# Kernel tuning notes

Measured on AMD Instinct MI355X. Metric: run time of the kernel, lower is better.

## Reference

```python
import jax, jax.numpy as jnp
import numpy as np

N_NODES = 20000
N_EDGES = 320000  # directed edges, in reverse pairs (2*i, 2*i+1)
F_NODE = 64
F_EDGE = 16
HID = 300
DEPTH = 3
N_GRAPHS = 128


def setup_inputs() -> dict:
    key = jax.random.key(0)
    ks = jax.random.split(key, 16)
    x = jax.random.normal(ks[0], (N_NODES, F_NODE), dtype=jnp.float32)
    edge_attr = jax.random.normal(ks[1], (N_EDGES, F_EDGE), dtype=jnp.float32)
    # build paired directed edges: edge 2*i is (src,dst), edge 2*i+1 is (dst,src)
    half = N_EDGES // 2
    src = jax.random.randint(ks[2], (half,), 0, N_NODES)
    dst = jax.random.randint(ks[3], (half,), 0, N_NODES)
    row = jnp.stack([src, dst], axis=1).reshape(-1)  # [E]
    col = jnp.stack([dst, src], axis=1).reshape(-1)  # [E]
    edge_index = jnp.stack([row, col], axis=0)  # [2, E]
    batch = jnp.sort(jax.random.randint(ks[4], (N_NODES,), 0, N_GRAPHS))
    s = 0.05
    W_init = jax.random.normal(ks[5], (F_NODE + F_EDGE, HID), dtype=jnp.float32) * s
    b_init = jnp.zeros((HID,), dtype=jnp.float32)
    W_convs = jax.random.normal(ks[6], (DEPTH, HID, HID), dtype=jnp.float32) * s
    b_convs = jnp.zeros((DEPTH, HID), dtype=jnp.float32)
    W_e2n = jax.random.normal(ks[7], (F_NODE + HID, HID), dtype=jnp.float32) * s
    b_e2n = jnp.zeros((HID,), dtype=jnp.float32)
    W_ffn = jax.random.normal(ks[8], (HID, 1), dtype=jnp.float32) * s
    b_ffn = jnp.zeros((1,), dtype=jnp.float32)
    return {"x": x, "edge_attr": edge_attr, "edge_index": edge_index, "batch": batch,
            "W_init": W_init, "b_init": b_init, "W_convs": W_convs, "b_convs": b_convs,
            "W_e2n": W_e2n, "b_e2n": b_e2n, "W_ffn": W_ffn, "b_ffn": b_ffn}


def _rev(h):
    # swap each consecutive forward/reverse edge pair
    e = h.shape[0]
    return h.reshape(e // 2, 2, -1)[:, ::-1, :].reshape(e, -1)


def reference(x, edge_attr, edge_index, batch, W_init, b_init, W_convs, b_convs,
              W_e2n, b_e2n, W_ffn, b_ffn):
    row, col = edge_index[0], edge_index[1]
    # h_0 = act(edge_init(cat([x[row], edge_attr])))
    h0 = jax.nn.relu(jnp.concatenate([x[row], edge_attr], axis=1) @ W_init + b_init)
    h = h0
    for l in range(DEPTH):
        # DMPNNConv: scatter-add edge features to target nodes, gather at source,
        # subtract reverse-edge message, apply Linear
        a = jax.ops.segment_sum(h, col, num_segments=N_NODES)  # [N, H]
        h = (a[row] - _rev(h)) @ W_convs[l] + b_convs[l]
        h = jax.nn.relu(h + h0)  # skip then activation; dropout is eval no-op
    # final conv's a_message only
    s = jax.ops.segment_sum(h, col, num_segments=N_NODES)  # [N, H]
    q = jnp.concatenate([x, s], axis=1)
    hn = jax.nn.relu(q @ W_e2n + b_e2n)  # [N, H]
    pooled = jax.ops.segment_sum(hn, batch, num_segments=N_GRAPHS)  # [G, H]
    return (pooled @ W_ffn + b_ffn).squeeze(-1)  # [G]
```

## Files before the change

kernel.cpp:

```cpp
#include <hip/hip_runtime.h>
#include <hip/hip_bf16.h>

typedef unsigned short ushort_t;
typedef __attribute__((ext_vector_type(8))) short short8;
typedef __attribute__((ext_vector_type(4))) float f32x4;
typedef __attribute__((ext_vector_type(2))) float f32x2;

#define N_NODES 20000
#define N_EDGES 320000
#define F_NODE 64
#define F_EDGE 16
#define HID 300
#define HP 300
#define NTILES 20
#define DEPTH 3
#define N_GRAPHS 128
#define KE2N 384
#define ATS 328

#define WFRAG_USHORT_PER_LAYER (10 * NTILES * 64 * 8)
#define W2FRAG_USHORT (NTILES * 64 * 8)
#define WE2NFRAG_USHORT (12 * NTILES * 64 * 8)

__device__ __forceinline__ float bf2f(ushort_t u) {
    union { unsigned int i; float f; } v;
    v.i = ((unsigned int)u) << 16;
    return v.f;
}

__device__ __forceinline__ f32x2 bfpair(unsigned int u) {
    union { unsigned int i[2]; f32x2 f; } v;
    v.i[0] = u << 16;
    v.i[1] = u & 0xffff0000u;
    return v.f;
}

__device__ __forceinline__ f32x2 pmax0(f32x2 a) {
#if __has_builtin(__builtin_elementwise_max)
    f32x2 z = {0.f, 0.f};
    return __builtin_elementwise_max(a, z);
#else
    f32x2 r; r.x = fmaxf(a.x, 0.f); r.y = fmaxf(a.y, 0.f); return r;
#endif
}

__device__ __forceinline__ unsigned int fpack(float lo, float hi) {
#if __has_builtin(__builtin_amdgcn_cvt_pk_bf16_f32)
    auto r = __builtin_amdgcn_cvt_pk_bf16_f32(lo, hi);
    union { decltype(r) b; unsigned int u; } v;
    v.b = r;
    return v.u;
#else
    union { float f; unsigned int i; } a, b;
    a.f = lo; b.f = hi;
    return ((a.i + 0x8000u) >> 16) | ((b.i + 0x8000u) & 0xffff0000u);
#endif
}
__device__ __forceinline__ unsigned int fpack2(f32x2 a) { return fpack(a.x, a.y); }
__device__ __forceinline__ ushort_t f2bf(float f) {
    return (ushort_t)(fpack(f, 0.f) & 0xffffu);
}

__global__ __launch_bounds__(256) void csr_hist(
    const int* __restrict__ col, int* __restrict__ deg)
{
    int e = blockIdx.x * 256 + threadIdx.x;
    atomicAdd(&deg[col[e]], 1);
}

__global__ __launch_bounds__(256) void csr_scan(
    const int* __restrict__ deg, int* __restrict__ offsets,
    int* __restrict__ cursor)
{
    __shared__ int sums[256];
    const int t = threadIdx.x;
    const int CH = 79;
    int base = t * CH;
    int local = 0;
    for (int i = 0; i < CH; ++i) {
        int idx = base + i;
        if (idx < N_NODES) local += deg[idx];
    }
    sums[t] = local;
    __syncthreads();
    for (int off = 1; off < 256; off <<= 1) {
        int v = (t >= off) ? sums[t - off] : 0;
        __syncthreads();
        sums[t] += v;
        __syncthreads();
    }
    int run = (t > 0) ? sums[t - 1] : 0;
    for (int i = 0; i < CH; ++i) {
        int idx = base + i;
        if (idx < N_NODES) {
            offsets[idx] = run;
            cursor[idx] = run;
            run += deg[idx];
        }
    }
}

__global__ __launch_bounds__(256) void csr_fill(
    const int* __restrict__ col, int* __restrict__ cursor,
    int* __restrict__ eid)
{
    int e = blockIdx.x * 256 + threadIdx.x;
    int pos = atomicAdd(&cursor[col[e]], 1);
    eid[pos] = e;
}

__global__ __launch_bounds__(256) void ghist(
    const int* __restrict__ batch, int* __restrict__ gdeg)
{
    int n = blockIdx.x * 256 + threadIdx.x;
    if (n < N_NODES) atomicAdd(&gdeg[batch[n]], 1);
}

__global__ __launch_bounds__(128) void gscan(
    const int* __restrict__ gdeg, int* __restrict__ goff)
{
    __shared__ int s[128];
    int t = threadIdx.x;
    int d = gdeg[t];
    s[t] = d;
    __syncthreads();
    for (int off = 1; off < 128; off <<= 1) {
        int v = (t >= off) ? s[t - off] : 0;
        __syncthreads();
        s[t] += v;
        __syncthreads();
    }
    goff[t] = s[t] - d;
    if (t == 127) goff[128] = s[127];
}

__global__ __launch_bounds__(64) void wfrag_build(
    const float* __restrict__ W_convs, ushort_t* __restrict__ wfrag)
{
    const int c = blockIdx.x, t = blockIdx.y, l = blockIdx.z;
    const int lane = threadIdx.x;
    const int k0 = c * 32 + (lane >> 4) * 8;
    const int n  = t * 16 + (lane & 15);
    ushort_t* dst = wfrag + (size_t)l * WFRAG_USHORT_PER_LAYER
                  + ((size_t)(c * NTILES + t) * 64 + lane) * 8;
    const float* Wl = W_convs + (size_t)l * HID * HID;
    #pragma unroll
    for (int j = 0; j < 8; ++j) {
        int k = k0 + j;
        float v = (k < HID && n < HID) ? Wl[(long)k * HID + n] : 0.f;
        dst[j] = f2bf(v);
    }
}

__global__ __launch_bounds__(64) void wfrag2_build(
    const float* __restrict__ W_e2n, ushort_t* __restrict__ wfrag2)
{
    const int c = blockIdx.x, t = blockIdx.y;
    const int lane = threadIdx.x;
    const int k0 = c * 32 + (lane >> 4) * 8;
    const int n  = t * 16 + (lane & 15);
    ushort_t* dst = wfrag2 + ((size_t)(c * NTILES + t) * 64 + lane) * 8;
    #pragma unroll
    for (int j = 0; j < 8; ++j) {
        int k = k0 + j;
        float v = (k < F_NODE + HID && n < HID) ? W_e2n[(long)k * HID + n] : 0.f;
        dst[j] = f2bf(v);
    }
}

__global__ __launch_bounds__(64) void w2frag_build(
    const float* __restrict__ W2, ushort_t* __restrict__ w2frag)
{
    const int t = blockIdx.x;
    const int lane = threadIdx.x;
    const int k0 = (lane >> 4) * 8;
    const int n  = t * 16 + (lane & 15);
    ushort_t* dst = w2frag + ((size_t)t * 64 + lane) * 8;
    #pragma unroll
    for (int j = 0; j < 8; ++j) {
        int k = k0 + j;
        float v = (k < F_EDGE && n < HID) ? W2[(long)k * HID + n] : 0.f;
        dst[j] = f2bf(v);
    }
}


__global__ __launch_bounds__(256) void node_init_gemm(
    const float* __restrict__ x, const float* __restrict__ W_init,
    const float* __restrict__ b_init, ushort_t* __restrict__ xW1b)
{
    __shared__ float xs[16 * 64];
    const int tid = threadIdx.x;
    const long n0 = (long)blockIdx.x * 16;
    for (int i = tid; i < 16 * 64; i += 256) xs[i] = x[n0 * 64 + i];
    __syncthreads();
    const int nl = tid >> 4, ct = tid & 15;
    for (int q = 0; q < 19; ++q) {
        int c = ct + 16 * q;
        if (c < HID) {
            float acc = b_init[c];
            #pragma unroll 8
            for (int k = 0; k < 64; ++k)
                acc = fmaf(xs[nl * 64 + k], W_init[(long)k * HID + c], acc);
            xW1b[(n0 + nl) * HID + c] = f2bf(acc);
        }
    }
}

template<bool UPDATE>
__global__ __launch_bounds__(256) void fused_conv(
    ushort_t* h, const ushort_t* __restrict__ Sb,
    const ushort_t* __restrict__ xW1b, const float* __restrict__ edge_attr,
    const int* __restrict__ row, const ushort_t* __restrict__ w2frag,
    const ushort_t* __restrict__ wfrag_l)
{
    __shared__ ushort_t At[32 * ATS];
    __shared__ int rows[32];
    const int tid = threadIdx.x;
    const int wave = tid >> 6, lane = tid & 63;
    const int quad = lane >> 4, m = lane & 15;
    const long e0 = (long)blockIdx.x * 32;
    if (tid < 32) rows[tid] = row[e0 + tid];

    {
        short8 a_ea[2];
        #pragma unroll
        for (int mt = 0; mt < 2; ++mt) {
            union { uint4 u4; short8 s8; } af;
            if (quad < 2) {
                const float* eap = edge_attr + (e0 + mt * 16 + m) * 16 + quad * 8;
                float4 v0 = *(const float4*)eap;
                float4 v1 = *(const float4*)(eap + 4);
                af.u4.x = fpack(v0.x, v0.y); af.u4.y = fpack(v0.z, v0.w);
                af.u4.z = fpack(v1.x, v1.y); af.u4.w = fpack(v1.z, v1.w);
            } else {
                af.u4.x = 0; af.u4.y = 0; af.u4.z = 0; af.u4.w = 0;
            }
            a_ea[mt] = af.s8;
        }
        const int nt0 = wave * 5;
        #pragma unroll
        for (int t = 0; t < 5; ++t) {
            short8 b = *(const short8*)(w2frag + ((size_t)(nt0 + t) * 64 + lane) * 8);
            int c = (nt0 + t) * 16 + m;
            #pragma unroll
            for (int mt = 0; mt < 2; ++mt) {
                f32x4 pc = (f32x4){0.f, 0.f, 0.f, 0.f};
                pc = __builtin_amdgcn_mfma_f32_16x16x32_bf16(a_ea[mt], b, pc, 0, 0, 0);
                #pragma unroll
                for (int r = 0; r < 4; ++r)
                    At[(mt * 16 + quad * 4 + r) * ATS + c] = f2bf(pc[r]);
            }
        }
    }
    __syncthreads();

    for (int i = tid; i < 16 * 80; i += 256) {
        int p = i / 80, g = i % 80;
        int c0 = 4 * g;
        int la = 2 * p, lb = 2 * p + 1;
        uint2 oa, ob;
        if (g < 75) {
            long Ea = e0 + la, Eb = e0 + lb;
            int ra = rows[la], rb = rows[lb];
            uint2 xa = *(const uint2*)&xW1b[(long)ra * HID + c0];
            uint2 xb = *(const uint2*)&xW1b[(long)rb * HID + c0];
            uint2 pa = *(const uint2*)&At[la * ATS + c0];
            uint2 pb = *(const uint2*)&At[lb * ATS + c0];
            f32x2 h0a0 = pmax0(bfpair(xa.x) + bfpair(pa.x));
            f32x2 h0a1 = pmax0(bfpair(xa.y) + bfpair(pa.y));
            f32x2 h0b0 = pmax0(bfpair(xb.x) + bfpair(pb.x));
            f32x2 h0b1 = pmax0(bfpair(xb.y) + bfpair(pb.y));
            if (UPDATE) {
                uint2 wa = *(const uint2*)&h[Ea * HP + c0];
                uint2 wb = *(const uint2*)&h[Eb * HP + c0];
                uint2 sa = *(const uint2*)&Sb[(long)ra * HID + c0];
                uint2 sb = *(const uint2*)&Sb[(long)rb * HID + c0];
                oa.x = fpack2(pmax0(bfpair(sa.x) - bfpair(wb.x) + h0a0));
                oa.y = fpack2(pmax0(bfpair(sa.y) - bfpair(wb.y) + h0a1));
                ob.x = fpack2(pmax0(bfpair(sb.x) - bfpair(wa.x) + h0b0));
                ob.y = fpack2(pmax0(bfpair(sb.y) - bfpair(wa.y) + h0b1));
            } else {
                oa.x = fpack2(h0a0); oa.y = fpack2(h0a1);
                ob.x = fpack2(h0b0); ob.y = fpack2(h0b1);
            }
        } else {
            oa.x = 0; oa.y = 0;
            ob = oa;
        }
        *(uint2*)&At[la * ATS + c0] = oa;
        *(uint2*)&At[lb * ATS + c0] = ob;
    }
    __syncthreads();

    const int nt0 = wave * 5;
    f32x4 acc[5][2];
    #pragma unroll
    for (int t = 0; t < 5; ++t)
        #pragma unroll
        for (int mt = 0; mt < 2; ++mt)
            acc[t][mt] = (f32x4){0.f, 0.f, 0.f, 0.f};

    for (int c = 0; c < 10; ++c) {
        short8 a[2];
        #pragma unroll
        for (int mt = 0; mt < 2; ++mt)
            a[mt] = *(const short8*)&At[(mt * 16 + m) * ATS + c * 32 + quad * 8];
        #pragma unroll
        for (int t = 0; t < 5; ++t) {
            short8 b = *(const short8*)(wfrag_l
                + ((size_t)(c * NTILES + nt0 + t) * 64 + lane) * 8);
            #pragma unroll
            for (int mt = 0; mt < 2; ++mt)
                acc[t][mt] = __builtin_amdgcn_mfma_f32_16x16x32_bf16(
                    a[mt], b, acc[t][mt], 0, 0, 0);
        }
    }
    #pragma unroll
    for (int t = 0; t < 5; ++t) {
        int col = (nt0 + t) * 16 + m;
        if (col >= HID) continue;
        #pragma unroll
        for (int mt = 0; mt < 2; ++mt) {
            long rbase = (e0 + mt * 16 + quad * 4) * HP + col;
            #pragma unroll
            for (int r = 0; r < 4; ++r)
                h[rbase + (long)r * HP] = f2bf(acc[t][mt][r]);
        }
    }
}

__global__ __launch_bounds__(256) void edge_update_mfma(
    ushort_t* h, const ushort_t* __restrict__ Sb,
    const ushort_t* __restrict__ xW1b, const float* __restrict__ edge_attr,
    const int* __restrict__ row, const ushort_t* __restrict__ w2frag)
{
    __shared__ ushort_t Pt[32 * ATS];
    __shared__ int rows[32];
    const int tid = threadIdx.x;
    const int wave = tid >> 6, lane = tid & 63;
    const int quad = lane >> 4, m = lane & 15;
    const long e0 = (long)blockIdx.x * 32;
    if (tid < 32) rows[tid] = row[e0 + tid];

    {
        short8 a_ea[2];
        #pragma unroll
        for (int mt = 0; mt < 2; ++mt) {
            union { uint4 u4; short8 s8; } af;
            if (quad < 2) {
                const float* eap = edge_attr + (e0 + mt * 16 + m) * 16 + quad * 8;
                float4 v0 = *(const float4*)eap;
                float4 v1 = *(const float4*)(eap + 4);
                af.u4.x = fpack(v0.x, v0.y); af.u4.y = fpack(v0.z, v0.w);
                af.u4.z = fpack(v1.x, v1.y); af.u4.w = fpack(v1.z, v1.w);
            } else {
                af.u4.x = 0; af.u4.y = 0; af.u4.z = 0; af.u4.w = 0;
            }
            a_ea[mt] = af.s8;
        }
        const int nt0 = wave * 5;
        #pragma unroll
        for (int t = 0; t < 5; ++t) {
            short8 b = *(const short8*)(w2frag + ((size_t)(nt0 + t) * 64 + lane) * 8);
            #pragma unroll
            for (int mt = 0; mt < 2; ++mt) {
                f32x4 pc = (f32x4){0.f, 0.f, 0.f, 0.f};
                pc = __builtin_amdgcn_mfma_f32_16x16x32_bf16(a_ea[mt], b, pc, 0, 0, 0);
                int c = (nt0 + t) * 16 + m;
                #pragma unroll
                for (int r = 0; r < 4; ++r)
                    Pt[(mt * 16 + quad * 4 + r) * ATS + c] = f2bf(pc[r]);
            }
        }
    }
    __syncthreads();

    for (int i = tid; i < 16 * 75; i += 256) {
        int p = i / 75, g = i % 75;
        int c0 = 4 * g;
        int la = 2 * p, lb = 2 * p + 1;
        long Ea = e0 + la, Eb = e0 + lb;
        int ra = rows[la], rb = rows[lb];
        uint2 wa = *(const uint2*)&h[Ea * HP + c0];
        uint2 wb = *(const uint2*)&h[Eb * HP + c0];
        uint2 sa = *(const uint2*)&Sb[(long)ra * HID + c0];
        uint2 sb = *(const uint2*)&Sb[(long)rb * HID + c0];
        uint2 xa = *(const uint2*)&xW1b[(long)ra * HID + c0];
        uint2 xb = *(const uint2*)&xW1b[(long)rb * HID + c0];
        uint2 pa = *(const uint2*)&Pt[la * ATS + c0];
        uint2 pb = *(const uint2*)&Pt[lb * ATS + c0];
        f32x2 h0a0 = pmax0(bfpair(xa.x) + bfpair(pa.x));
        f32x2 h0a1 = pmax0(bfpair(xa.y) + bfpair(pa.y));
        f32x2 h0b0 = pmax0(bfpair(xb.x) + bfpair(pb.x));
        f32x2 h0b1 = pmax0(bfpair(xb.y) + bfpair(pb.y));
        uint2 oa, ob;
        oa.x = fpack2(pmax0(bfpair(sa.x) - bfpair(wb.x) + h0a0));
        oa.y = fpack2(pmax0(bfpair(sa.y) - bfpair(wb.y) + h0a1));
        ob.x = fpack2(pmax0(bfpair(sb.x) - bfpair(wa.x) + h0b0));
        ob.y = fpack2(pmax0(bfpair(sb.y) - bfpair(wa.y) + h0b1));
        *(uint2*)&h[Ea * HP + c0] = oa;
        *(uint2*)&h[Eb * HP + c0] = ob;
    }
}

__global__ __launch_bounds__(256) void gather_sum(
    const ushort_t* __restrict__ src, const int* __restrict__ offsets,
    const int* __restrict__ ends, const int* __restrict__ eid,
    const float* __restrict__ bias, ushort_t* __restrict__ Sb)
{
    long idx = (long)blockIdx.x * 256 + threadIdx.x;
    if (idx >= (long)N_NODES * 75) return;
    int n = (int)(idx / 75);
    int g = (int)(idx % 75);
    int beg = offsets[n], end = ends[n];
    f32x2 A0 = {0.f, 0.f}, A1 = {0.f, 0.f};
    f32x2 B0 = {0.f, 0.f}, B1 = {0.f, 0.f};
    int j = beg;
    for (; j + 1 < end; j += 2) {
        int e0i = eid[j], e1i = eid[j + 1];
        uint2 v0 = ((const uint2*)src)[(long)e0i * (HP / 4) + g];
        uint2 v1 = ((const uint2*)src)[(long)e1i * (HP / 4) + g];
        A0 += bfpair(v0.x); A1 += bfpair(v0.y);
        B0 += bfpair(v1.x); B1 += bfpair(v1.y);
    }
    if (j < end) {
        int e0i = eid[j];
        uint2 v0 = ((const uint2*)src)[(long)e0i * (HP / 4) + g];
        A0 += bfpair(v0.x); A1 += bfpair(v0.y);
    }
    float4 bv = *(const float4*)&bias[4 * g];
    f32x2 bv0 = {bv.x, bv.y}, bv1 = {bv.z, bv.w};
    uint2 o;
    o.x = fpack2(A0 + B0 + bv0);
    o.y = fpack2(A1 + B1 + bv1);
    *(uint2*)&Sb[(long)n * HID + 4 * g] = o;
}

__global__ __launch_bounds__(256) void gather_ab(
    const ushort_t* __restrict__ src, const int* __restrict__ offsets,
    const int* __restrict__ ends, const int* __restrict__ eid,
    ushort_t* __restrict__ Ab)
{
    long idx = (long)blockIdx.x * 256 + threadIdx.x;
    if (idx >= (long)N_NODES * 75) return;
    int n = (int)(idx / 75);
    int g = (int)(idx % 75);
    int beg = offsets[n], end = ends[n];
    f32x2 A0 = {0.f, 0.f}, A1 = {0.f, 0.f};
    f32x2 B0 = {0.f, 0.f}, B1 = {0.f, 0.f};
    int j = beg;
    for (; j + 1 < end; j += 2) {
        int e0i = eid[j], e1i = eid[j + 1];
        uint2 v0 = ((const uint2*)src)[(long)e0i * (HP / 4) + g];
        uint2 v1 = ((const uint2*)src)[(long)e1i * (HP / 4) + g];
        A0 += bfpair(v0.x); A1 += bfpair(v0.y);
        B0 += bfpair(v1.x); B1 += bfpair(v1.y);
    }
    if (j < end) {
        int e0i = eid[j];
        uint2 v0 = ((const uint2*)src)[(long)e0i * (HP / 4) + g];
        A0 += bfpair(v0.x); A1 += bfpair(v0.y);
    }
    uint2 o;
    o.x = fpack2(A0 + B0);
    o.y = fpack2(A1 + B1);
    *(uint2*)&Ab[(long)n * KE2N + 64 + 4 * g] = o;
}

__global__ __launch_bounds__(256) void x_fill(
    const float* __restrict__ x, ushort_t* __restrict__ Ab)
{
    long idx = (long)blockIdx.x * 256 + threadIdx.x;
    if (idx >= (long)N_NODES * 21) return;
    int n = (int)(idx / 21);
    int q = (int)(idx % 21);
    if (q < 16) {
        float4 v = *(const float4*)&x[(long)n * 64 + 4 * q];
        uint2 o;
        o.x = fpack(v.x, v.y);
        o.y = fpack(v.z, v.w);
        *(uint2*)&Ab[(long)n * KE2N + 4 * q] = o;
    } else {
        uint2 o; o.x = 0; o.y = 0;
        *(uint2*)&Ab[(long)n * KE2N + 364 + 4 * (q - 16)] = o;
    }
}

__global__ __launch_bounds__(256) void e2n_mfma(
    const ushort_t* __restrict__ Ab, const ushort_t* __restrict__ wfrag2,
    const float* __restrict__ b_e2n, float* __restrict__ hn)
{
    const int tid = threadIdx.x;
    const int wave = tid >> 6, lane = tid & 63;
    const int quad = lane >> 4, m = lane & 15;
    const long n0 = (long)blockIdx.x * 64;
    const int nt0 = wave * 5;

    f32x4 acc[5][4];
    #pragma unroll
    for (int t = 0; t < 5; ++t)
        #pragma unroll
        for (int mt = 0; mt < 4; ++mt)
            acc[t][mt] = (f32x4){0.f, 0.f, 0.f, 0.f};

    for (int c = 0; c < 12; ++c) {
        short8 a[4];
        #pragma unroll
        for (int mt = 0; mt < 4; ++mt) {
            long r = n0 + mt * 16 + m;
            if (r > N_NODES - 1) r = N_NODES - 1;
            a[mt] = *(const short8*)(Ab + r * KE2N + c * 32 + quad * 8);
        }
        #pragma unroll
        for (int t = 0; t < 5; ++t) {
            short8 b = *(const short8*)(wfrag2
                + ((size_t)(c * NTILES + nt0 + t) * 64 + lane) * 8);
            #pragma unroll
            for (int mt = 0; mt < 4; ++mt)
                acc[t][mt] = __builtin_amdgcn_mfma_f32_16x16x32_bf16(
                    a[mt], b, acc[t][mt], 0, 0, 0);
        }
    }

    #pragma unroll
    for (int t = 0; t < 5; ++t) {
        int col = (nt0 + t) * 16 + m;
        if (col >= HID) continue;
        float bias = b_e2n[col];
        #pragma unroll
        for (int mt = 0; mt < 4; ++mt) {
            long rw = n0 + mt * 16 + quad * 4;
            #pragma unroll
            for (int r = 0; r < 4; ++r) {
                long rowi = rw + r;
                if (rowi < N_NODES)
                    hn[rowi * HP + col] = fmaxf(acc[t][mt][r] + bias, 0.f);
            }
        }
    }
}

__global__ __launch_bounds__(256) void pool_graph(
    const float* __restrict__ hn, const int* __restrict__ goff,
    float* __restrict__ pooled)
{
    int g = blockIdx.x;
    int beg = goff[g], end = goff[g + 1];
    for (int c = threadIdx.x; c < HID; c += 256) {
        float acc = 0.f;
        for (int n = beg; n < end; ++n)
            acc += hn[(long)n * HP + c];
        pooled[(long)g * HID + c] = acc;
    }
}

__global__ __launch_bounds__(64) void ffn_out(
    const float* __restrict__ pooled, const float* __restrict__ W_ffn,
    const float* __restrict__ b_ffn, float* __restrict__ out)
{
    int g = blockIdx.x;
    int lane = threadIdx.x;
    float s = 0.f;
    for (int c = lane; c < HID; c += 64)
        s += pooled[(long)g * HID + c] * W_ffn[c];
    #pragma unroll
    for (int off = 32; off > 0; off >>= 1)
        s += __shfl_down(s, off, 64);
    if (lane == 0) out[g] = s + b_ffn[0];
}

extern "C" void kernel_launch(void* const* d_in, const int* in_sizes, int n_in,
                              void* d_out, int out_size, void* d_ws, size_t ws_size,
                              hipStream_t stream) {
    const float* x         = (const float*)d_in[0];
    const float* edge_attr = (const float*)d_in[1];
    const int*   edge_index= (const int*)d_in[2];
    const int*   batch     = (const int*)d_in[3];
    const float* W_init    = (const float*)d_in[4];
    const float* b_init    = (const float*)d_in[5];
    const float* W_convs   = (const float*)d_in[6];
    const float* b_convs   = (const float*)d_in[7];
    const float* W_e2n     = (const float*)d_in[8];
    const float* b_e2n     = (const float*)d_in[9];
    const float* W_ffn     = (const float*)d_in[10];
    const float* b_ffn     = (const float*)d_in[11];
    float* out = (float*)d_out;

    const int* row = edge_index;
    const int* col = edge_index + N_EDGES;
    const float* W2 = W_init + (size_t)F_NODE * HID;

    const size_t need = (size_t)N_EDGES * HP * 2
                      + (size_t)N_NODES * HID * 2
                      + (size_t)N_NODES * KE2N * 2
                      + (size_t)N_GRAPHS * HID * 4
                      + (size_t)N_NODES * 4 * 2 + (size_t)N_EDGES * 4
                      + (size_t)DEPTH * WFRAG_USHORT_PER_LAYER * 2
                      + (size_t)WE2NFRAG_USHORT * 2
                      + (size_t)W2FRAG_USHORT * 2
                      + (size_t)(N_GRAPHS + 1 + N_GRAPHS) * 4 + 32768;
    if (ws_size < need) return;

    char* p = (char*)d_ws;
    auto take = [&](size_t bytes) {
        char* q = p;
        p += (bytes + 255) & ~(size_t)255;
        return q;
    };
    ushort_t* h       = (ushort_t*)take((size_t)N_EDGES * HP * 2);
    ushort_t* Sb      = (ushort_t*)take((size_t)N_NODES * HID * 2);
    ushort_t* Ab      = (ushort_t*)take((size_t)N_NODES * KE2N * 2);
    float*    pooled  = (float*)take((size_t)N_GRAPHS * HID * 4);
    int*      cursor  = (int*)take((size_t)N_NODES * 4);
    int*      offsets = (int*)take((size_t)N_NODES * 4);
    int*      eid     = (int*)take((size_t)N_EDGES * 4);
    ushort_t* wfrag   = (ushort_t*)take((size_t)DEPTH * WFRAG_USHORT_PER_LAYER * 2);
    ushort_t* wfrag2  = (ushort_t*)take((size_t)WE2NFRAG_USHORT * 2);
    ushort_t* w2frag  = (ushort_t*)take((size_t)W2FRAG_USHORT * 2);
    int*      gdeg    = (int*)take((size_t)N_GRAPHS * 4);
    int*      goff    = (int*)take((size_t)(N_GRAPHS + 1) * 4);

    ushort_t* xW1b = Ab;
    float*    hn   = (float*)h;

    hipMemsetAsync(cursor, 0, (size_t)N_NODES * 4, stream);
    hipMemsetAsync(gdeg, 0, (size_t)N_GRAPHS * 4, stream);
    csr_hist<<<N_EDGES / 256, 256, 0, stream>>>(col, cursor);
    csr_scan<<<1, 256, 0, stream>>>(cursor, offsets, cursor);
    csr_fill<<<N_EDGES / 256, 256, 0, stream>>>(col, cursor, eid);
    ghist<<<(N_NODES + 255) / 256, 256, 0, stream>>>(batch, gdeg);
    gscan<<<1, 128, 0, stream>>>(gdeg, goff);

    wfrag_build<<<dim3(10, NTILES, DEPTH), 64, 0, stream>>>(W_convs, wfrag);
    wfrag2_build<<<dim3(12, NTILES, 1), 64, 0, stream>>>(W_e2n, wfrag2);
    w2frag_build<<<NTILES, 64, 0, stream>>>(W2, w2frag);

    node_init_gemm<<<N_NODES / 16, 256, 0, stream>>>(x, W_init, b_init, xW1b);

    const int GS_GRID = ((N_NODES * 75) + 255) / 256;

    fused_conv<false><<<N_EDGES / 32, 256, 0, stream>>>(
        h, Sb, xW1b, edge_attr, row, w2frag, wfrag);
    gather_sum<<<GS_GRID, 256, 0, stream>>>(
        h, offsets, cursor, eid, b_convs + 0 * HID, Sb);
    fused_conv<true><<<N_EDGES / 32, 256, 0, stream>>>(
        h, Sb, xW1b, edge_attr, row, w2frag,
        wfrag + 1 * (size_t)WFRAG_USHORT_PER_LAYER);
    gather_sum<<<GS_GRID, 256, 0, stream>>>(
        h, offsets, cursor, eid, b_convs + 1 * HID, Sb);
    fused_conv<true><<<N_EDGES / 32, 256, 0, stream>>>(
        h, Sb, xW1b, edge_attr, row, w2frag,
        wfrag + 2 * (size_t)WFRAG_USHORT_PER_LAYER);
    gather_sum<<<GS_GRID, 256, 0, stream>>>(
        h, offsets, cursor, eid, b_convs + 2 * HID, Sb);
    edge_update_mfma<<<N_EDGES / 32, 256, 0, stream>>>(
        h, Sb, xW1b, edge_attr, row, w2frag);

    x_fill<<<((N_NODES * 21) + 255) / 256, 256, 0, stream>>>(x, Ab);
    gather_ab<<<GS_GRID, 256, 0, stream>>>(h, offsets, cursor, eid, Ab);
    e2n_mfma<<<(N_NODES + 63) / 64, 256, 0, stream>>>(Ab, wfrag2, b_e2n, hn);
    pool_graph<<<N_GRAPHS, 256, 0, stream>>>(hn, goff, pooled);
    ffn_out<<<N_GRAPHS, 64, 0, stream>>>(pooled, W_ffn, b_ffn, out);
}
```

Measured before the change: 1.233 ms.

## Software-pipeline gathers and MFMA operand loads; widen edge update and gather unroll

In fused_conv, the row/xW1b/h/Sb gathers for each elementwise iteration are issued one step ahead, and the first batch is issued before the edge-attr MFMA phase so its latency overlaps that compute. The main MFMA loop double-buffers its weight and LDS operand fragments. edge_update_mfma moves to 512 threads, using 8 waves for the edge-attr projection and the same prefetched gather scheme. The gather_sum and gather_ab kernels unroll their edge loops by 4 with separate accumulators to raise memory-level parallelism. The cost is higher register pressure, which could reduce occupancy.

```diff
diff --git a/kernel.cpp b/kernel.cpp
--- a/kernel.cpp
+++ b/kernel.cpp
@@ -207,6 +207,41 @@
     }
 }
 
+__device__ __forceinline__ void p_phase8(
+    ushort_t* At, const float* __restrict__ edge_attr,
+    const ushort_t* __restrict__ w2frag, long e0,
+    int wave, int quad, int m, int lane)
+{
+    const int mtp = wave >> 2;
+    const int nt0p = (wave & 3) * 5;
+    short8 a_ea;
+    {
+        union { uint4 u4; short8 s8; } af;
+        if (quad < 2) {
+            const float* eap = edge_attr + (e0 + mtp * 16 + m) * 16 + quad * 8;
+            float4 v0 = *(const float4*)eap;
+            float4 v1 = *(const float4*)(eap + 4);
+            af.u4.x = fpack(v0.x, v0.y); af.u4.y = fpack(v0.z, v0.w);
+            af.u4.z = fpack(v1.x, v1.y); af.u4.w = fpack(v1.z, v1.w);
+        } else {
+            af.u4.x = 0; af.u4.y = 0; af.u4.z = 0; af.u4.w = 0;
+        }
+        a_ea = af.s8;
+    }
+    #pragma unroll
+    for (int t = 0; t < 5; ++t) {
+        int nt = nt0p + t;
+        if (nt >= 19) continue;
+        short8 b = *(const short8*)(w2frag + ((size_t)nt * 64 + lane) * 8);
+        int c = nt * 16 + m;
+        f32x4 pc = (f32x4){0.f, 0.f, 0.f, 0.f};
+        pc = __builtin_amdgcn_mfma_f32_16x16x32_bf16(a_ea, b, pc, 0, 0, 0);
+        #pragma unroll
+        for (int r = 0; r < 4; ++r)
+            At[(mtp * 16 + quad * 4 + r) * ATS + c] = f2bf(pc[r]);
+    }
+}
+
 template<bool UPDATE>
 __global__ __launch_bounds__(256) void fused_conv(
     ushort_t* h, const ushort_t* __restrict__ Sb,
@@ -215,12 +250,33 @@
     const ushort_t* __restrict__ wfrag_l)
 {
     __shared__ ushort_t At[32 * ATS];
-    __shared__ int rows[32];
     const int tid = threadIdx.x;
     const int wave = tid >> 6, lane = tid & 63;
     const int quad = lane >> 4, m = lane & 15;
     const long e0 = (long)blockIdx.x * 32;
-    if (tid < 32) rows[tid] = row[e0 + tid];
+
+    auto issue = [&](int k, uint2& xa, uint2& xb, uint2& wa, uint2& wb,
+                     uint2& sa, uint2& sb, int& la, int& lb, int& g) {
+        int i = tid + (k << 8);
+        int p = i / 80; g = i % 80;
+        la = 2 * p; lb = la + 1;
+        if (g < 75) {
+            int c0 = 4 * g;
+            int ra = row[e0 + la], rb = row[e0 + lb];
+            xa = *(const uint2*)&xW1b[(long)ra * HID + c0];
+            xb = *(const uint2*)&xW1b[(long)rb * HID + c0];
+            if (UPDATE) {
+                wa = *(const uint2*)&h[(e0 + la) * HP + c0];
+                wb = *(const uint2*)&h[(e0 + lb) * HP + c0];
+                sa = *(const uint2*)&Sb[(long)ra * HID + c0];
+                sb = *(const uint2*)&Sb[(long)rb * HID + c0];
+            }
+        }
+    };
+
+    uint2 xa0, xb0, wa0, wb0, sa0, sb0;
+    int la0, lb0, g0;
+    issue(0, xa0, xb0, wa0, wb0, sa0, sb0, la0, lb0, g0);
 
     {
         short8 a_ea[2];
@@ -255,31 +311,26 @@
     }
     __syncthreads();
 
-    for (int i = tid; i < 16 * 80; i += 256) {
-        int p = i / 80, g = i % 80;
-        int c0 = 4 * g;
-        int la = 2 * p, lb = 2 * p + 1;
+    #pragma unroll
+    for (int k = 0; k < 5; ++k) {
+        uint2 xa1, xb1, wa1, wb1, sa1, sb1;
+        int la1 = 0, lb1 = 0, g1 = 0;
+        if (k < 4)
+            issue(k + 1, xa1, xb1, wa1, wb1, sa1, sb1, la1, lb1, g1);
+        int c0 = 4 * g0;
         uint2 oa, ob;
-        if (g < 75) {
-            long Ea = e0 + la, Eb = e0 + lb;
-            int ra = rows[la], rb = rows[lb];
-            uint2 xa = *(const uint2*)&xW1b[(long)ra * HID + c0];
-            uint2 xb = *(const uint2*)&xW1b[(long)rb * HID + c0];
-            uint2 pa = *(const uint2*)&At[la * ATS + c0];
-            uint2 pb = *(const uint2*)&At[lb * ATS + c0];
-            f32x2 h0a0 = pmax0(bfpair(xa.x) + bfpair(pa.x));
-            f32x2 h0a1 = pmax0(bfpair(xa.y) + bfpair(pa.y));
-            f32x2 h0b0 = pmax0(bfpair(xb.x) + bfpair(pb.x));
-            f32x2 h0b1 = pmax0(bfpair(xb.y) + bfpair(pb.y));
+        if (g0 < 75) {
+            uint2 pa = *(const uint2*)&At[la0 * ATS + c0];
+            uint2 pb = *(const uint2*)&At[lb0 * ATS + c0];
+            f32x2 h0a0 = pmax0(bfpair(xa0.x) + bfpair(pa.x));
+            f32x2 h0a1 = pmax0(bfpair(xa0.y) + bfpair(pa.y));
+            f32x2 h0b0 = pmax0(bfpair(xb0.x) + bfpair(pb.x));
+            f32x2 h0b1 = pmax0(bfpair(xb0.y) + bfpair(pb.y));
             if (UPDATE) {
-                uint2 wa = *(const uint2*)&h[Ea * HP + c0];
-                uint2 wb = *(const uint2*)&h[Eb * HP + c0];
-                uint2 sa = *(const uint2*)&Sb[(long)ra * HID + c0];
-                uint2 sb = *(const uint2*)&Sb[(long)rb * HID + c0];
-                oa.x = fpack2(pmax0(bfpair(sa.x) - bfpair(wb.x) + h0a0));
-                oa.y = fpack2(pmax0(bfpair(sa.y) - bfpair(wb.y) + h0a1));
-                ob.x = fpack2(pmax0(bfpair(sb.x) - bfpair(wa.x) + h0b0));
-                ob.y = fpack2(pmax0(bfpair(sb.y) - bfpair(wa.y) + h0b1));
+                oa.x = fpack2(pmax0(bfpair(sa0.x) - bfpair(wb0.x) + h0a0));
+                oa.y = fpack2(pmax0(bfpair(sa0.y) - bfpair(wb0.y) + h0a1));
+                ob.x = fpack2(pmax0(bfpair(sb0.x) - bfpair(wa0.x) + h0b0));
+                ob.y = fpack2(pmax0(bfpair(sb0.y) - bfpair(wa0.y) + h0b1));
             } else {
                 oa.x = fpack2(h0a0); oa.y = fpack2(h0a1);
                 ob.x = fpack2(h0b0); ob.y = fpack2(h0b1);
@@ -288,8 +339,12 @@
             oa.x = 0; oa.y = 0;
             ob = oa;
         }
-        *(uint2*)&At[la * ATS + c0] = oa;
-        *(uint2*)&At[lb * ATS + c0] = ob;
+        *(uint2*)&At[la0 * ATS + c0] = oa;
+        *(uint2*)&At[lb0 * ATS + c0] = ob;
+        if (k < 4) {
+            xa0 = xa1; xb0 = xb1; wa0 = wa1; wb0 = wb1;
+            sa0 = sa1; sb0 = sb1; la0 = la1; lb0 = lb1; g0 = g1;
+        }
     }
     __syncthreads();
 
@@ -301,19 +356,37 @@
         for (int mt = 0; mt < 2; ++mt)
             acc[t][mt] = (f32x4){0.f, 0.f, 0.f, 0.f};
 
+    short8 bc[5], ac[2];
+    #pragma unroll
+    for (int t = 0; t < 5; ++t)
+        bc[t] = *(const short8*)(wfrag_l + ((size_t)(nt0 + t) * 64 + lane) * 8);
+    #pragma unroll
+    for (int mt = 0; mt < 2; ++mt)
+        ac[mt] = *(const short8*)&At[(mt * 16 + m) * ATS + quad * 8];
+
+    #pragma unroll
     for (int c = 0; c < 10; ++c) {
-        short8 a[2];
-        #pragma unroll
-        for (int mt = 0; mt < 2; ++mt)
-            a[mt] = *(const short8*)&At[(mt * 16 + m) * ATS + c * 32 + quad * 8];
-        #pragma unroll
-        for (int t = 0; t < 5; ++t) {
-            short8 b = *(const short8*)(wfrag_l
-                + ((size_t)(c * NTILES + nt0 + t) * 64 + lane) * 8);
+        short8 bn[5], an[2];
+        if (c < 9) {
+            #pragma unroll
+            for (int t = 0; t < 5; ++t)
+                bn[t] = *(const short8*)(wfrag_l
+                    + ((size_t)((c + 1) * NTILES + nt0 + t) * 64 + lane) * 8);
+            #pragma unroll
+            for (int mt = 0; mt < 2; ++mt)
+                an[mt] = *(const short8*)&At[(mt * 16 + m) * ATS
+                    + (c + 1) * 32 + quad * 8];
+        }
+        #pragma unroll
+        for (int t = 0; t < 5; ++t)
             #pragma unroll
             for (int mt = 0; mt < 2; ++mt)
                 acc[t][mt] = __builtin_amdgcn_mfma_f32_16x16x32_bf16(
-                    a[mt], b, acc[t][mt], 0, 0, 0);
+                    ac[mt], bc[t], acc[t][mt], 0, 0, 0);
+        if (c < 9) {
+            #pragma unroll
+            for (int t = 0; t < 5; ++t) bc[t] = bn[t];
+            ac[0] = an[0]; ac[1] = an[1];
         }
     }
     #pragma unroll
@@ -330,77 +403,68 @@
     }
 }
 
-__global__ __launch_bounds__(256) void edge_update_mfma(
+__global__ __launch_bounds__(512) void edge_update_mfma(
     ushort_t* h, const ushort_t* __restrict__ Sb,
     const ushort_t* __restrict__ xW1b, const float* __restrict__ edge_attr,
     const int* __restrict__ row, const ushort_t* __restrict__ w2frag)
 {
     __shared__ ushort_t Pt[32 * ATS];
-    __shared__ int rows[32];
     const int tid = threadIdx.x;
     const int wave = tid >> 6, lane = tid & 63;
     const int quad = lane >> 4, m = lane & 15;
     const long e0 = (long)blockIdx.x * 32;
-    if (tid < 32) rows[tid] = row[e0 + tid];
-
-    {
-        short8 a_ea[2];
-        #pragma unroll
-        for (int mt = 0; mt < 2; ++mt) {
-            union { uint4 u4; short8 s8; } af;
-            if (quad < 2) {
-                const float* eap = edge_attr + (e0 + mt * 16 + m) * 16 + quad * 8;
-                float4 v0 = *(const float4*)eap;
-                float4 v1 = *(const float4*)(eap + 4);
-                af.u4.x = fpack(v0.x, v0.y); af.u4.y = fpack(v0.z, v0.w);
-                af.u4.z = fpack(v1.x, v1.y); af.u4.w = fpack(v1.z, v1.w);
-            } else {
-                af.u4.x = 0; af.u4.y = 0; af.u4.z = 0; af.u4.w = 0;
-            }
-            a_ea[mt] = af.s8;
-        }
-        const int nt0 = wave * 5;
-        #pragma unroll
-        for (int t = 0; t < 5; ++t) {
-            short8 b = *(const short8*)(w2frag + ((size_t)(nt0 + t) * 64 + lane) * 8);
-            #pragma unroll
-            for (int mt = 0; mt < 2; ++mt) {
-                f32x4 pc = (f32x4){0.f, 0.f, 0.f, 0.f};
-                pc = __builtin_amdgcn_mfma_f32_16x16x32_bf16(a_ea[mt], b, pc, 0, 0, 0);
-                int c = (nt0 + t) * 16 + m;
-                #pragma unroll
-                for (int r = 0; r < 4; ++r)
-                    Pt[(mt * 16 + quad * 4 + r) * ATS + c] = f2bf(pc[r]);
-            }
-        }
-    }
+
+    auto issue = [&](int k, uint2& xa, uint2& xb, uint2& wa, uint2& wb,
+                     uint2& sa, uint2& sb, int& la, int& lb, int& g, bool& v) {
+        int i = tid + (k << 9);
+        v = i < 16 * 75;
+        if (v) {
+            int p = i / 75; g = i % 75;
+            la = 2 * p; lb = la + 1;
+            int c0 = 4 * g;
+            int ra = row[e0 + la], rb = row[e0 + lb];
+            xa = *(const uint2*)&xW1b[(long)ra * HID + c0];
+            xb = *(const uint2*)&xW1b[(long)rb * HID + c0];
+            wa = *(const uint2*)&h[(e0 + la) * HP + c0];
+            wb = *(const uint2*)&h[(e0 + lb) * HP + c0];
+            sa = *(const uint2*)&Sb[(long)ra * HID + c0];
+            sb = *(const uint2*)&Sb[(long)rb * HID + c0];
+        }
+    };
+
+    uint2 xa0, xb0, wa0, wb0, sa0, sb0;
+    int la0 = 0, lb0 = 0, g0 = 0; bool v0 = false;
+    issue(0, xa0, xb0, wa0, wb0, sa0, sb0, la0, lb0, g0, v0);
+
+    p_phase8(Pt, edge_attr, w2frag, e0, wave, quad, m, lane);
     __syncthreads();
 
-    for (int i = tid; i < 16 * 75; i += 256) {
-        int p = i / 75, g = i % 75;
-        int c0 = 4 * g;
-        int la = 2 * p, lb = 2 * p + 1;
-        long Ea = e0 + la, Eb = e0 + lb;
-        int ra = rows[la], rb = rows[lb];
-        uint2 wa = *(const uint2*)&h[Ea * HP + c0];
-        uint2 wb = *(const uint2*)&h[Eb * HP + c0];
-        uint2 sa = *(const uint2*)&Sb[(long)ra * HID + c0];
-        uint2 sb = *(const uint2*)&Sb[(long)rb * HID + c0];
-        uint2 xa = *(const uint2*)&xW1b[(long)ra * HID + c0];
-        uint2 xb = *(const uint2*)&xW1b[(long)rb * HID + c0];
-        uint2 pa = *(const uint2*)&Pt[la * ATS + c0];
-        uint2 pb = *(const uint2*)&Pt[lb * ATS + c0];
-        f32x2 h0a0 = pmax0(bfpair(xa.x) + bfpair(pa.x));
-        f32x2 h0a1 = pmax0(bfpair(xa.y) + bfpair(pa.y));
-        f32x2 h0b0 = pmax0(bfpair(xb.x) + bfpair(pb.x));
-        f32x2 h0b1 = pmax0(bfpair(xb.y) + bfpair(pb.y));
-        uint2 oa, ob;
-        oa.x = fpack2(pmax0(bfpair(sa.x) - bfpair(wb.x) + h0a0));
-        oa.y = fpack2(pmax0(bfpair(sa.y) - bfpair(wb.y) + h0a1));
-        ob.x = fpack2(pmax0(bfpair(sb.x) - bfpair(wa.x) + h0b0));
-        ob.y = fpack2(pmax0(bfpair(sb.y) - bfpair(wa.y) + h0b1));
-        *(uint2*)&h[Ea * HP + c0] = oa;
-        *(uint2*)&h[Eb * HP + c0] = ob;
+    #pragma unroll
+    for (int k = 0; k < 3; ++k) {
+        uint2 xa1, xb1, wa1, wb1, sa1, sb1;
+        int la1 = 0, lb1 = 0, g1 = 0; bool v1 = false;
+        if (k < 2)
+            issue(k + 1, xa1, xb1, wa1, wb1, sa1, sb1, la1, lb1, g1, v1);
+        if (v0) {
+            int c0 = 4 * g0;
+            uint2 pa = *(const uint2*)&Pt[la0 * ATS + c0];
+            uint2 pb = *(const uint2*)&Pt[lb0 * ATS + c0];
+            f32x2 h0a0 = pmax0(bfpair(xa0.x) + bfpair(pa.x));
+            f32x2 h0a1 = pmax0(bfpair(xa0.y) + bfpair(pa.y));
+            f32x2 h0b0 = pmax0(bfpair(xb0.x) + bfpair(pb.x));
+            f32x2 h0b1 = pmax0(bfpair(xb0.y) + bfpair(pb.y));
+            uint2 oa, ob;
+            oa.x = fpack2(pmax0(bfpair(sa0.x) - bfpair(wb0.x) + h0a0));
+            oa.y = fpack2(pmax0(bfpair(sa0.y) - bfpair(wb0.y) + h0a1));
+            ob.x = fpack2(pmax0(bfpair(sb0.x) - bfpair(wa0.x) + h0b0));
+            ob.y = fpack2(pmax0(bfpair(sb0.y) - bfpair(wa0.y) + h0b1));
+            *(uint2*)&h[(e0 + la0) * HP + c0] = oa;
+            *(uint2*)&h[(e0 + lb0) * HP + c0] = ob;
+        }
+        if (k < 2) {
+            xa0 = xa1; xb0 = xb1; wa0 = wa1; wb0 = wb1;
+            sa0 = sa1; sb0 = sb1; la0 = la1; lb0 = lb1; g0 = g1; v0 = v1;
+        }
     }
 }
 
@@ -416,24 +480,30 @@
     int beg = offsets[n], end = ends[n];
     f32x2 A0 = {0.f, 0.f}, A1 = {0.f, 0.f};
     f32x2 B0 = {0.f, 0.f}, B1 = {0.f, 0.f};
+    f32x2 C0 = {0.f, 0.f}, C1 = {0.f, 0.f};
+    f32x2 D0 = {0.f, 0.f}, D1 = {0.f, 0.f};
     int j = beg;
-    for (; j + 1 < end; j += 2) {
-        int e0i = eid[j], e1i = eid[j + 1];
-        uint2 v0 = ((const uint2*)src)[(long)e0i * (HP / 4) + g];
-        uint2 v1 = ((const uint2*)src)[(long)e1i * (HP / 4) + g];
-        A0 += bfpair(v0.x); A1 += bfpair(v0.y);
-        B0 += bfpair(v1.x); B1 += bfpair(v1.y);
-    }
-    if (j < end) {
-        int e0i = eid[j];
-        uint2 v0 = ((const uint2*)src)[(long)e0i * (HP / 4) + g];
-        A0 += bfpair(v0.x); A1 += bfpair(v0.y);
+    for (; j + 3 < end; j += 4) {
+        int ea = eid[j], eb = eid[j + 1], ec = eid[j + 2], ed = eid[j + 3];
+        uint2 va = ((const uint2*)src)[(long)ea * (HP / 4) + g];
+        uint2 vb = ((const uint2*)src)[(long)eb * (HP / 4) + g];
+        uint2 vc = ((const uint2*)src)[(long)ec * (HP / 4) + g];
+        uint2 vd = ((const uint2*)src)[(long)ed * (HP / 4) + g];
+        A0 += bfpair(va.x); A1 += bfpair(va.y);
+        B0 += bfpair(vb.x); B1 += bfpair(vb.y);
+        C0 += bfpair(vc.x); C1 += bfpair(vc.y);
+        D0 += bfpair(vd.x); D1 += bfpair(vd.y);
+    }
+    for (; j < end; ++j) {
+        int ea = eid[j];
+        uint2 va = ((const uint2*)src)[(long)ea * (HP / 4) + g];
+        A0 += bfpair(va.x); A1 += bfpair(va.y);
     }
     float4 bv = *(const float4*)&bias[4 * g];
     f32x2 bv0 = {bv.x, bv.y}, bv1 = {bv.z, bv.w};
     uint2 o;
-    o.x = fpack2(A0 + B0 + bv0);
-    o.y = fpack2(A1 + B1 + bv1);
+    o.x = fpack2((A0 + B0) + (C0 + D0) + bv0);
+    o.y = fpack2((A1 + B1) + (C1 + D1) + bv1);
     *(uint2*)&Sb[(long)n * HID + 4 * g] = o;
 }
 
@@ -449,22 +519,28 @@
     int beg = offsets[n], end = ends[n];
     f32x2 A0 = {0.f, 0.f}, A1 = {0.f, 0.f};
     f32x2 B0 = {0.f, 0.f}, B1 = {0.f, 0.f};
+    f32x2 C0 = {0.f, 0.f}, C1 = {0.f, 0.f};
+    f32x2 D0 = {0.f, 0.f}, D1 = {0.f, 0.f};
     int j = beg;
-    for (; j + 1 < end; j += 2) {
-        int e0i = eid[j], e1i = eid[j + 1];
-        uint2 v0 = ((const uint2*)src)[(long)e0i * (HP / 4) + g];
-        uint2 v1 = ((const uint2*)src)[(long)e1i * (HP / 4) + g];
-        A0 += bfpair(v0.x); A1 += bfpair(v0.y);
-        B0 += bfpair(v1.x); B1 += bfpair(v1.y);
-    }
-    if (j < end) {
-        int e0i = eid[j];
-        uint2 v0 = ((const uint2*)src)[(long)e0i * (HP / 4) + g];
-        A0 += bfpair(v0.x); A1 += bfpair(v0.y);
+    for (; j + 3 < end; j += 4) {
+        int ea = eid[j], eb = eid[j + 1], ec = eid[j + 2], ed = eid[j + 3];
+        uint2 va = ((const uint2*)src)[(long)ea * (HP / 4) + g];
+        uint2 vb = ((const uint2*)src)[(long)eb * (HP / 4) + g];
+        uint2 vc = ((const uint2*)src)[(long)ec * (HP / 4) + g];
+        uint2 vd = ((const uint2*)src)[(long)ed * (HP / 4) + g];
+        A0 += bfpair(va.x); A1 += bfpair(va.y);
+        B0 += bfpair(vb.x); B1 += bfpair(vb.y);
+        C0 += bfpair(vc.x); C1 += bfpair(vc.y);
+        D0 += bfpair(vd.x); D1 += bfpair(vd.y);
+    }
+    for (; j < end; ++j) {
+        int ea = eid[j];
+        uint2 va = ((const uint2*)src)[(long)ea * (HP / 4) + g];
+        A0 += bfpair(va.x); A1 += bfpair(va.y);
     }
     uint2 o;
-    o.x = fpack2(A0 + B0);
-    o.y = fpack2(A1 + B1);
+    o.x = fpack2((A0 + B0) + (C0 + D0));
+    o.y = fpack2((A1 + B1) + (C1 + D1));
     *(uint2*)&Ab[(long)n * KE2N + 64 + 4 * g] = o;
 }
 
@@ -654,7 +730,7 @@
         wfrag + 2 * (size_t)WFRAG_USHORT_PER_LAYER);
     gather_sum<<<GS_GRID, 256, 0, stream>>>(
         h, offsets, cursor, eid, b_convs + 2 * HID, Sb);
-    edge_update_mfma<<<N_EDGES / 32, 256, 0, stream>>>(
+    edge_update_mfma<<<N_EDGES / 32, 512, 0, stream>>>(
         h, Sb, xW1b, edge_attr, row, w2frag);
 
     x_fill<<<((N_NODES * 21) + 255) / 256, 256, 0, stream>>>(x, Ab);
```

New measurement: 1.285 ms. 1.04x slower.
